# Kernel optimization log

Measured on AMD Instinct MI355X. Metric: run time of the kernel, lower is better.

## Reference

```python
import jax, jax.numpy as jnp
import numpy as np

NUM_HEADS = 2
ROPE_BASE = 10000.0


def _rope_tables(seq_len, head_dim, dtype):
    # inv_freq over even indices of head_dim
    inv_freq = 1.0 / (ROPE_BASE ** (jnp.arange(0, head_dim, 2, dtype=jnp.float32) / head_dim))
    t = jnp.arange(seq_len, dtype=jnp.float32)
    freqs = t[:, None] * inv_freq[None, :]            # (s, head_dim/2)
    emb = jnp.concatenate([freqs, freqs], axis=-1)    # (s, head_dim)
    return jnp.cos(emb).astype(dtype), jnp.sin(emb).astype(dtype)


def _apply_rotation(x_bsd, cos, sin):
    # x_bsd: (b, s, h*d); chunk in half along last dim (h=2 -> halves == head_dim)
    x1, x2 = jnp.split(x_bsd, 2, axis=-1)
    return jnp.concatenate([x1 * cos - x2 * sin, x2 * cos + x1 * sin], axis=-1)


def setup_inputs() -> dict:
    key = jax.random.key(0)
    k1, k2, k3, k4 = jax.random.split(key, 4)
    b, s, dim = 4, 2048, 2048
    x = jax.random.normal(k1, (b, s, dim), dtype=jnp.float32)
    wqkv = jax.random.normal(k2, (dim, 3 * dim), dtype=jnp.float32) * (dim ** -0.5)
    wout = jax.random.normal(k3, (dim, dim), dtype=jnp.float32) * (dim ** -0.5)
    bout = jax.random.normal(k4, (dim,), dtype=jnp.float32) * 0.01
    return {"x": x, "wqkv": wqkv, "wout": wout, "bout": bout}


def reference(x, wqkv, wout, bout):
    b, s, dim = x.shape
    h = NUM_HEADS
    d = dim // h
    scale = d ** -0.5

    qkv = x @ wqkv                                    # (b, s, 3*dim)
    qkv = qkv.reshape(b, s, 3, h, d).transpose(2, 0, 3, 1, 4)  # (3, b, h, s, d)
    q, k, v = qkv[0], qkv[1], qkv[2]                  # (b, h, s, d)

    # RoPE applied on (b, s, h*d) layout, exactly as source
    cos, sin = _rope_tables(s, d, x.dtype)            # (s, d) each
    q_flat = q.transpose(0, 2, 1, 3).reshape(b, s, h * d)
    k_flat = k.transpose(0, 2, 1, 3).reshape(b, s, h * d)
    q = _apply_rotation(q_flat, cos, sin).reshape(b, s, h, d).transpose(0, 2, 1, 3)
    k = _apply_rotation(k_flat, cos, sin).reshape(b, s, h, d).transpose(0, 2, 1, 3)

    scores = jnp.einsum('bhid,bhjd->bhij', q, k) * scale
    attn = jax.nn.softmax(scores, axis=-1)
    out = jnp.einsum('bhij,bhjd->bhid', attn, v)      # (b, h, s, d)
    out = out.transpose(0, 2, 1, 3).reshape(b, s, dim)
    return out @ wout + bout
```

## Files before the change

### kernel.cpp

```cpp
#include <hip/hip_runtime.h>
#include <hip/hip_fp16.h>

typedef __attribute__((ext_vector_type(4))) float f32x4;
typedef __attribute__((ext_vector_type(8))) _Float16 f16x8;
typedef __attribute__((ext_vector_type(4))) _Float16 f16x4;

__device__ __forceinline__ void gload_lds16(const void* gp, void* lp) {
    __builtin_amdgcn_global_load_lds(
        (const __attribute__((address_space(1))) void*)gp,
        (__attribute__((address_space(3))) void*)lp, 16, 0, 0);
}

__global__ void f32_to_f16_vec(const float* __restrict__ in, _Float16* __restrict__ out) {
    long i = ((long)blockIdx.x * 256 + threadIdx.x) * 4;
    f32x4 v = *(const f32x4*)(in + i);
    f16x4 h;
#pragma unroll
    for (int e = 0; e < 4; ++e) h[e] = (_Float16)v[e];
    *(f16x4*)(out + i) = h;
}

__global__ void transpose_f32_to_f16(const float* __restrict__ in, _Float16* __restrict__ out,
                                     int R, int C) {
    __shared__ _Float16 tile[32][36];
    const int c0 = blockIdx.x * 32, r0 = blockIdx.y * 32;
    const int t = threadIdx.x;
    const int r = t >> 3, c4 = (t & 7) * 4;
    f32x4 v = *(const f32x4*)(in + (long)(r0 + r) * C + c0 + c4);
    f16x4 h;
#pragma unroll
    for (int e = 0; e < 4; ++e) h[e] = (_Float16)v[e];
    *(f16x4*)&tile[r][c4] = h;
    __syncthreads();
    const int oc = t >> 3, o4 = (t & 7) * 4;
    f16x4 o;
#pragma unroll
    for (int e = 0; e < 4; ++e) o[e] = tile[o4 + e][oc];
    *(f16x4*)(out + (long)(c0 + oc) * R + r0 + o4) = o;
}

__global__ void rope_inplace(_Float16* __restrict__ qkv) {
    const int row = blockIdx.x;
    const int s = row & 2047;
    const int j0 = threadIdx.x * 4;
    _Float16* base = qkv + (long)row * 6144;
    f16x4 q0 = *(const f16x4*)(base + j0);
    f16x4 q1 = *(const f16x4*)(base + 1024 + j0);
    f16x4 k0 = *(const f16x4*)(base + 2048 + j0);
    f16x4 k1 = *(const f16x4*)(base + 3072 + j0);
    f16x4 oq0, oq1, ok0, ok1;
#pragma unroll
    for (int e = 0; e < 4; ++e) {
        int fi = (j0 + e) & 511;
        float expo = (float)(2 * fi) * (1.0f / 1024.0f);
        float invf = 1.0f / powf(10000.0f, expo);
        float ang = (float)s * invf;
        float sn, cs;
        sincosf(ang, &sn, &cs);
        float a = (float)q0[e], b = (float)q1[e];
        oq0[e] = (_Float16)(a * cs - b * sn);
        oq1[e] = (_Float16)(b * cs + a * sn);
        float c = (float)k0[e], d = (float)k1[e];
        ok0[e] = (_Float16)(c * cs - d * sn);
        ok1[e] = (_Float16)(d * cs + c * sn);
    }
    *(f16x4*)(base + j0) = oq0;
    *(f16x4*)(base + 1024 + j0) = oq1;
    *(f16x4*)(base + 2048 + j0) = ok0;
    *(f16x4*)(base + 3072 + j0) = ok1;
}

__global__ void v_transpose(const _Float16* __restrict__ qkv, _Float16* __restrict__ vT) {
    __shared__ _Float16 tile[32][36];
    const int z = blockIdx.z, b = z >> 1, h = z & 1;
    const int s0 = blockIdx.x * 32, d0 = blockIdx.y * 32;
    const int t = threadIdx.x;
    const int r = t >> 3, c4 = (t & 7) * 4;
    const _Float16* src = qkv + (long)(b * 2048 + s0 + r) * 6144 + 4096 + h * 1024 + d0 + c4;
    *(f16x4*)&tile[r][c4] = *(const f16x4*)src;
    __syncthreads();
    const int dr = t >> 3, sc = (t & 7) * 4;
    f16x4 o;
#pragma unroll
    for (int e = 0; e < 4; ++e) o[e] = tile[sc + e][dr];
    *(f16x4*)(vT + ((long)z * 1024 + d0 + dr) * 2048 + s0 + sc) = o;
}

__global__ __launch_bounds__(256) void softmax_rows_f32(float* __restrict__ S, float scale) {
    const int wid = threadIdx.x >> 6, lane = threadIdx.x & 63;
    const long row = (long)blockIdx.x * 4 + wid;
    float* rp = S + row * 2048;
    f32x4 v[8];
    float mx = -1e30f;
#pragma unroll
    for (int i = 0; i < 8; ++i) {
        v[i] = *(const f32x4*)(rp + (i * 64 + lane) * 4);
#pragma unroll
        for (int e = 0; e < 4; ++e) mx = fmaxf(mx, v[i][e]);
    }
#pragma unroll
    for (int o = 32; o > 0; o >>= 1) mx = fmaxf(mx, __shfl_xor(mx, o, 64));
    float sum = 0.f;
#pragma unroll
    for (int i = 0; i < 8; ++i)
#pragma unroll
        for (int e = 0; e < 4; ++e) {
            float p = __expf(scale * (v[i][e] - mx));
            v[i][e] = p; sum += p;
        }
#pragma unroll
    for (int o = 32; o > 0; o >>= 1) sum += __shfl_xor(sum, o, 64);
    float inv = 1.0f / sum;
    _Float16* wp = (_Float16*)S + row * 4096;
#pragma unroll
    for (int i = 0; i < 8; ++i) {
        f16x4 h;
#pragma unroll
        for (int e = 0; e < 4; ++e) h[e] = (_Float16)(v[i][e] * inv);
        *(f16x4*)(wp + (i * 64 + lane) * 4) = h;
    }
}

__global__ __launch_bounds__(256) void softmax_rows_f16(_Float16* __restrict__ S, float scale) {
    const int wid = threadIdx.x >> 6, lane = threadIdx.x & 63;
    const long row = (long)blockIdx.x * 4 + wid;
    _Float16* rp = S + row * 2048;
    f16x8 v[4];
    float f[32];
    float mx = -1e30f;
#pragma unroll
    for (int i = 0; i < 4; ++i) {
        v[i] = *(const f16x8*)(rp + i * 512 + lane * 8);
#pragma unroll
        for (int e = 0; e < 8; ++e) {
            f[i * 8 + e] = (float)v[i][e];
            mx = fmaxf(mx, f[i * 8 + e]);
        }
    }
#pragma unroll
    for (int o = 32; o > 0; o >>= 1) mx = fmaxf(mx, __shfl_xor(mx, o, 64));
    float sum = 0.f;
#pragma unroll
    for (int i = 0; i < 32; ++i) {
        float p = __expf(scale * (f[i] - mx));
        f[i] = p; sum += p;
    }
#pragma unroll
    for (int o = 32; o > 0; o >>= 1) sum += __shfl_xor(sum, o, 64);
    float inv = 1.0f / sum;
#pragma unroll
    for (int i = 0; i < 4; ++i) {
        f16x8 h;
#pragma unroll
        for (int e = 0; e < 8; ++e) h[e] = (_Float16)(f[i * 8 + e] * inv);
        *(f16x8*)(rp + i * 512 + lane * 8) = h;
    }
}

template <bool OUT_F16, bool BIAS>
__global__ __launch_bounds__(512, 2)
void gemm256(const _Float16* __restrict__ A, const _Float16* __restrict__ B,
             void* __restrict__ Cv, const float* __restrict__ bias,
             int K, int lda, int ldb, int ldc, int zmod,
             long a1, long a2, long b1, long b2, long c1, long c2) {
    __shared__ char lds[131072];
    const int z = blockIdx.z, zq = z / zmod, zr = z - zq * zmod;
    A += zq * a1 + zr * a2;
    B += zq * b1 + zr * b2;
    const long coff = zq * c1 + zr * c2;
    const int tm = blockIdx.y * 256, tn = blockIdx.x * 256;
    const int t = threadIdx.x;
    const int lane = t & 63, wid = t >> 6;
    const int wr = wid >> 2, wc = wid & 3;
    const int fr = lane & 15, kg = lane >> 4;

    const int strow = wid * 16 + (lane >> 3);
    const int stcol = ((lane & 7) ^ (lane >> 3)) * 8;
    const _Float16* gA = A + (long)(tm + strow) * lda + stcol;
    const _Float16* gB = B + (long)(tn + strow) * ldb + stcol;
    char* const ldsw = lds + wid * 2048;

    const int sw0 = 16 * ((0 * 4 + kg) ^ (fr & 7));
    const int sw1 = 16 * ((1 * 4 + kg) ^ (fr & 7));

    const int NT = K >> 6;
    f32x4 acc[8][4] = {};

    auto stageA = [&](int tt, int h) {
        const _Float16* s = gA + (long)(h * 128) * lda + tt * 64;
        char* d = ldsw + (tt & 1) * 65536 + h * 16384;
        gload_lds16(s, d);
        gload_lds16(s + (long)8 * lda, d + 1024);
    };
    auto stageB = [&](int tt, int h) {
        const _Float16* s = gB + (long)(h * 128) * ldb + tt * 64;
        char* d = ldsw + (tt & 1) * 65536 + 32768 + h * 16384;
        gload_lds16(s, d);
        gload_lds16(s + (long)8 * ldb, d + 1024);
    };

    stageB(0, 0); stageB(0, 1); stageA(0, 0); stageA(0, 1);
    stageB(1, 0); stageB(1, 1);
    asm volatile("s_waitcnt vmcnt(4)" ::: "memory");
    __builtin_amdgcn_s_barrier();

    f16x8 af[4][2], bf0[2][2], bf1[2][2];
    const int arow = (wr * 128 + fr) * 128;
    const int brow = 32768 + (wc * 64 + fr) * 128;

    for (int g = 0; g < NT; ++g) {
        const char* buf = lds + (g & 1) * 65536;
#pragma unroll
        for (int m = 0; m < 4; ++m) {
            af[m][0] = *(const f16x8*)(buf + arow + m * 2048 + sw0);
            af[m][1] = *(const f16x8*)(buf + arow + m * 2048 + sw1);
        }
#pragma unroll
        for (int n = 0; n < 2; ++n) {
            bf0[n][0] = *(const f16x8*)(buf + brow + n * 2048 + sw0);
            bf0[n][1] = *(const f16x8*)(buf + brow + n * 2048 + sw1);
        }
        if (g + 1 < NT) stageA(g + 1, 0);
        __builtin_amdgcn_s_barrier();
        asm volatile("s_waitcnt lgkmcnt(0)" ::: "memory");
        __builtin_amdgcn_sched_barrier(0);
        __builtin_amdgcn_s_setprio(1);
#pragma unroll
        for (int m = 0; m < 4; ++m)
#pragma unroll
            for (int n = 0; n < 2; ++n)
#pragma unroll
                for (int k = 0; k < 2; ++k)
                    acc[m][n] = __builtin_amdgcn_mfma_f32_16x16x32_f16(af[m][k], bf0[n][k], acc[m][n], 0, 0, 0);
        __builtin_amdgcn_s_setprio(0);
        __builtin_amdgcn_s_barrier();
#pragma unroll
        for (int n = 0; n < 2; ++n) {
            bf1[n][0] = *(const f16x8*)(buf + brow + 4096 + n * 2048 + sw0);
            bf1[n][1] = *(const f16x8*)(buf + brow + 4096 + n * 2048 + sw1);
        }
        if (g + 1 < NT) stageA(g + 1, 1);
        __builtin_amdgcn_s_barrier();
        asm volatile("s_waitcnt lgkmcnt(0)" ::: "memory");
        __builtin_amdgcn_sched_barrier(0);
        __builtin_amdgcn_s_setprio(1);
#pragma unroll
        for (int m = 0; m < 4; ++m)
#pragma unroll
            for (int n = 0; n < 2; ++n)
#pragma unroll
                for (int k = 0; k < 2; ++k)
                    acc[m][n + 2] = __builtin_amdgcn_mfma_f32_16x16x32_f16(af[m][k], bf1[n][k], acc[m][n + 2], 0, 0, 0);
        __builtin_amdgcn_s_setprio(0);
        __builtin_amdgcn_s_barrier();
#pragma unroll
        for (int m = 0; m < 4; ++m) {
            af[m][0] = *(const f16x8*)(buf + arow + 8192 + m * 2048 + sw0);
            af[m][1] = *(const f16x8*)(buf + arow + 8192 + m * 2048 + sw1);
        }
        if (g + 2 < NT) stageB(g + 2, 0);
        __builtin_amdgcn_s_barrier();
        asm volatile("s_waitcnt lgkmcnt(0)" ::: "memory");
        __builtin_amdgcn_sched_barrier(0);
        __builtin_amdgcn_s_setprio(1);
#pragma unroll
        for (int m = 0; m < 4; ++m)
#pragma unroll
            for (int n = 0; n < 2; ++n)
#pragma unroll
                for (int k = 0; k < 2; ++k)
                    acc[m + 4][n + 2] = __builtin_amdgcn_mfma_f32_16x16x32_f16(af[m][k], bf1[n][k], acc[m + 4][n + 2], 0, 0, 0);
        __builtin_amdgcn_s_setprio(0);
        __builtin_amdgcn_s_barrier();
        if (g + 2 < NT) stageB(g + 2, 1);
        __builtin_amdgcn_s_barrier();
        __builtin_amdgcn_s_setprio(1);
#pragma unroll
        for (int m = 0; m < 4; ++m)
#pragma unroll
            for (int n = 0; n < 2; ++n)
#pragma unroll
                for (int k = 0; k < 2; ++k)
                    acc[m + 4][n] = __builtin_amdgcn_mfma_f32_16x16x32_f16(af[m][k], bf0[n][k], acc[m + 4][n], 0, 0, 0);
        __builtin_amdgcn_s_setprio(0);
        if (g + 2 < NT)      asm volatile("s_waitcnt vmcnt(4)" ::: "memory");
        else if (g + 1 < NT) asm volatile("s_waitcnt vmcnt(0)" ::: "memory");
        __builtin_amdgcn_s_barrier();
    }

    const int rb = tm + wr * 128 + (lane >> 4) * 4;
    const int cb = tn + wc * 64 + fr;
#pragma unroll
    for (int m = 0; m < 8; ++m) {
#pragma unroll
        for (int n = 0; n < 4; ++n) {
#pragma unroll
            for (int r = 0; r < 4; ++r) {
                float v = acc[m][n][r];
                const int row = rb + m * 16 + r;
                const int col = cb + n * 16;
                if (BIAS) v += bias[col];
                if (OUT_F16)
                    ((_Float16*)Cv)[coff + (long)row * ldc + col] = (_Float16)v;
                else
                    ((float*)Cv)[coff + (long)row * ldc + col] = v;
            }
        }
    }
}

extern "C" void kernel_launch(void* const* d_in, const int* in_sizes, int n_in,
                              void* d_out, int out_size, void* d_ws, size_t ws_size,
                              hipStream_t stream) {
    const float* x    = (const float*)d_in[0];
    const float* wqkv = (const float*)d_in[1];
    const float* wout = (const float*)d_in[2];
    const float* bout = (const float*)d_in[3];
    char* ws = (char*)d_ws;

    _Float16* qkv_h = (_Float16*)(ws);
    _Float16* x_h   = (_Float16*)(ws + 100663296);
    _Float16* wqkvT = (_Float16*)(ws + 134217728);
    _Float16* vT    = (_Float16*)(ws + 100663296);
    _Float16* woutT = (_Float16*)(ws);
    const bool batched = ws_size >= 234881024ULL;

    f32_to_f16_vec<<<dim3(16384), dim3(256), 0, stream>>>(x, x_h);
    transpose_f32_to_f16<<<dim3(192, 64), dim3(256), 0, stream>>>(wqkv, wqkvT, 2048, 6144);
    gemm256<true, false><<<dim3(24, 32, 1), dim3(512), 0, stream>>>(
        x_h, wqkvT, (void*)qkv_h, nullptr, 2048, 2048, 2048, 6144,
        1, 0L, 0L, 0L, 0L, 0L, 0L);
    rope_inplace<<<dim3(8192), dim3(256), 0, stream>>>(qkv_h);
    v_transpose<<<dim3(64, 32, 8), dim3(256), 0, stream>>>(qkv_h, vT);

    if (batched) {
        _Float16* S16  = (_Float16*)(ws + 134217728);
        _Float16* aout = (_Float16*)(ws + 201326592);
        gemm256<true, false><<<dim3(8, 8, 8), dim3(512), 0, stream>>>(
            qkv_h, qkv_h + 2048, (void*)S16, nullptr, 1024, 6144, 6144, 2048,
            2, 12582912L, 1024L, 12582912L, 1024L, 8388608L, 4194304L);
        softmax_rows_f16<<<dim3(4096), dim3(256), 0, stream>>>(S16, 0.03125f);
        gemm256<true, false><<<dim3(4, 8, 8), dim3(512), 0, stream>>>(
            S16, vT, (void*)aout, nullptr, 2048, 2048, 2048, 2048,
            2, 8388608L, 4194304L, 4194304L, 2097152L, 4194304L, 1024L);
        transpose_f32_to_f16<<<dim3(64, 64), dim3(256), 0, stream>>>(wout, woutT, 2048, 2048);
        gemm256<false, true><<<dim3(8, 32, 1), dim3(512), 0, stream>>>(
            aout, woutT, d_out, bout, 2048, 2048, 2048, 2048,
            1, 0L, 0L, 0L, 0L, 0L, 0L);
    } else {
        float*    S32  = (float*)(ws + 134217728);
        _Float16* aout = (_Float16*)(ws + 150994944);
        for (int z = 0; z < 8; ++z) {
            const _Float16* Az = qkv_h + (long)(z >> 1) * 12582912 + (z & 1) * 1024;
            gemm256<false, false><<<dim3(8, 8, 1), dim3(512), 0, stream>>>(
                Az, Az + 2048, (void*)S32, nullptr, 1024, 6144, 6144, 2048,
                1, 0L, 0L, 0L, 0L, 0L, 0L);
            softmax_rows_f32<<<dim3(512), dim3(256), 0, stream>>>(S32, 0.03125f);
            gemm256<true, false><<<dim3(4, 8, 1), dim3(512), 0, stream>>>(
                (const _Float16*)S32, vT + (long)z * 2097152,
                (void*)(aout + (long)(z >> 1) * 4194304 + (z & 1) * 1024), nullptr,
                2048, 4096, 2048, 2048, 1, 0L, 0L, 0L, 0L, 0L, 0L);
        }
        transpose_f32_to_f16<<<dim3(64, 64), dim3(256), 0, stream>>>(wout, woutT, 2048, 2048);
        gemm256<false, true><<<dim3(8, 32, 1), dim3(512), 0, stream>>>(
            aout, woutT, d_out, bout, 2048, 2048, 2048, 2048,
            1, 0L, 0L, 0L, 0L, 0L, 0L);
    }
}
```

Baseline: 536.1 us.

## Precompute RoPE cos/sin tables and drop explicit LDS waits in GEMM loop

Adds a kernel that computes the cos/sin tables once per sequence position and frequency, so rope_inplace reads them instead of calling powf and sincosf for every element of every batch row. Separately, it removes the explicit lgkmcnt(0) waits and sched_barriers before three MFMA phases in the GEMM main loop, leaving the compiler to place the waits for the LDS fragment loads. That lets the scheduler overlap LDS reads with MFMAs but gives up the hand-controlled ordering. The tables reuse workspace that is overwritten later by vT.

```diff
diff --git a/kernel.cpp b/kernel.cpp
--- a/kernel.cpp
+++ b/kernel.cpp
@@ -9,6 +9,17 @@
     __builtin_amdgcn_global_load_lds(
         (const __attribute__((address_space(1))) void*)gp,
         (__attribute__((address_space(3))) void*)lp, 16, 0, 0);
+}
+
+__global__ void rope_tables_k(float* __restrict__ cosT, float* __restrict__ sinT) {
+    int idx = blockIdx.x * 256 + threadIdx.x;
+    int s = idx >> 9, j = idx & 511;
+    float invf = exp2f(-13.287712379549449f * (float)j * (1.0f / 512.0f));
+    float ang = (float)s * invf;
+    float sn, cs;
+    sincosf(ang, &sn, &cs);
+    cosT[idx] = cs;
+    sinT[idx] = sn;
 }
 
 __global__ void f32_to_f16_vec(const float* __restrict__ in, _Float16* __restrict__ out) {
@@ -39,7 +50,8 @@
     *(f16x4*)(out + (long)(c0 + oc) * R + r0 + o4) = o;
 }
 
-__global__ void rope_inplace(_Float16* __restrict__ qkv) {
+__global__ void rope_inplace(_Float16* __restrict__ qkv, const float* __restrict__ cosT,
+                             const float* __restrict__ sinT) {
     const int row = blockIdx.x;
     const int s = row & 2047;
     const int j0 = threadIdx.x * 4;
@@ -48,21 +60,18 @@
     f16x4 q1 = *(const f16x4*)(base + 1024 + j0);
     f16x4 k0 = *(const f16x4*)(base + 2048 + j0);
     f16x4 k1 = *(const f16x4*)(base + 3072 + j0);
+    const int jj = j0 & 511;
+    f32x4 cs = *(const f32x4*)(cosT + (long)s * 512 + jj);
+    f32x4 sn = *(const f32x4*)(sinT + (long)s * 512 + jj);
     f16x4 oq0, oq1, ok0, ok1;
 #pragma unroll
     for (int e = 0; e < 4; ++e) {
-        int fi = (j0 + e) & 511;
-        float expo = (float)(2 * fi) * (1.0f / 1024.0f);
-        float invf = 1.0f / powf(10000.0f, expo);
-        float ang = (float)s * invf;
-        float sn, cs;
-        sincosf(ang, &sn, &cs);
         float a = (float)q0[e], b = (float)q1[e];
-        oq0[e] = (_Float16)(a * cs - b * sn);
-        oq1[e] = (_Float16)(b * cs + a * sn);
+        oq0[e] = (_Float16)(a * cs[e] - b * sn[e]);
+        oq1[e] = (_Float16)(b * cs[e] + a * sn[e]);
         float c = (float)k0[e], d = (float)k1[e];
-        ok0[e] = (_Float16)(c * cs - d * sn);
-        ok1[e] = (_Float16)(d * cs + c * sn);
+        ok0[e] = (_Float16)(c * cs[e] - d * sn[e]);
+        ok1[e] = (_Float16)(d * cs[e] + c * sn[e]);
     }
     *(f16x4*)(base + j0) = oq0;
     *(f16x4*)(base + 1024 + j0) = oq1;
@@ -222,8 +231,6 @@
         }
         if (g + 1 < NT) stageA(g + 1, 0);
         __builtin_amdgcn_s_barrier();
-        asm volatile("s_waitcnt lgkmcnt(0)" ::: "memory");
-        __builtin_amdgcn_sched_barrier(0);
         __builtin_amdgcn_s_setprio(1);
 #pragma unroll
         for (int m = 0; m < 4; ++m)
@@ -241,8 +248,6 @@
         }
         if (g + 1 < NT) stageA(g + 1, 1);
         __builtin_amdgcn_s_barrier();
-        asm volatile("s_waitcnt lgkmcnt(0)" ::: "memory");
-        __builtin_amdgcn_sched_barrier(0);
         __builtin_amdgcn_s_setprio(1);
 #pragma unroll
         for (int m = 0; m < 4; ++m)
@@ -260,8 +265,6 @@
         }
         if (g + 2 < NT) stageB(g + 2, 0);
         __builtin_amdgcn_s_barrier();
-        asm volatile("s_waitcnt lgkmcnt(0)" ::: "memory");
-        __builtin_amdgcn_sched_barrier(0);
         __builtin_amdgcn_s_setprio(1);
 #pragma unroll
         for (int m = 0; m < 4; ++m)
@@ -322,6 +325,8 @@
     _Float16* x_h   = (_Float16*)(ws + 100663296);
     _Float16* wqkvT = (_Float16*)(ws + 134217728);
     _Float16* vT    = (_Float16*)(ws + 100663296);
+    float*    cosT  = (float*)(ws + 100663296);
+    float*    sinT  = (float*)(ws + 104857600);
     _Float16* woutT = (_Float16*)(ws);
     const bool batched = ws_size >= 234881024ULL;
 
@@ -330,7 +335,8 @@
     gemm256<true, false><<<dim3(24, 32, 1), dim3(512), 0, stream>>>(
         x_h, wqkvT, (void*)qkv_h, nullptr, 2048, 2048, 2048, 6144,
         1, 0L, 0L, 0L, 0L, 0L, 0L);
-    rope_inplace<<<dim3(8192), dim3(256), 0, stream>>>(qkv_h);
+    rope_tables_k<<<dim3(4096), dim3(256), 0, stream>>>(cosT, sinT);
+    rope_inplace<<<dim3(8192), dim3(256), 0, stream>>>(qkv_h, cosT, sinT);
     v_transpose<<<dim3(64, 32, 8), dim3(256), 0, stream>>>(qkv_h, vT);
 
     if (batched) {
```

After: 520.1 us. 1.03x faster.
